# Kernel tuning notes

Measured on AMD Instinct MI355X. Metric: run time of the kernel, lower is better.

## Reference

```python
import jax, jax.numpy as jnp
import numpy as np

B, N, DIM, H = 16, 197, 768, 12
HD = DIM // H
SCALE = HD ** -0.5
T = 4 * B * N          # uncompressed new-token stream from the 4 frames
M = B * N + T          # cache tokens + new tokens (gather source length)
INNER = 64             # restoration MLP inner dim
FF = 4 * DIM

def _ln(x, g, b, eps=1e-5):
    m = jnp.mean(x, axis=-1, keepdims=True)
    v = jnp.var(x, axis=-1, keepdims=True)
    return (x - m) * jax.lax.rsqrt(v + eps) * g + b

def _quick_gelu(x):
    return x * jax.nn.sigmoid(1.702 * x)

def setup_inputs():
    key = jax.random.key(0)
    ks = jax.random.split(key, 16)
    s = 0.02
    return {
        'list_hidden_states': jax.random.normal(ks[0], (1, T, DIM), jnp.float32),
        'diff_pre_proj': jax.random.normal(ks[1], (4, B, N, DIM), jnp.float32),
        'hqkv_cache': jax.random.normal(ks[2], (4, B, N, DIM), jnp.float32),
        'ln1_g': jnp.ones((DIM,), jnp.float32), 'ln1_b': jnp.zeros((DIM,), jnp.float32),
        'wq': jax.random.normal(ks[3], (DIM, DIM), jnp.float32) * s, 'bq': jnp.zeros((DIM,), jnp.float32),
        'wk': jax.random.normal(ks[4], (DIM, DIM), jnp.float32) * s, 'bk': jnp.zeros((DIM,), jnp.float32),
        'wv': jax.random.normal(ks[5], (DIM, DIM), jnp.float32) * s, 'bv': jnp.zeros((DIM,), jnp.float32),
        'rest_w1': jax.random.normal(ks[6], (DIM, INNER), jnp.float32) * s,
        'rest_w2': jax.random.normal(ks[7], (INNER, 4 * DIM), jnp.float32) * s,
        'wo': jax.random.normal(ks[8], (DIM, DIM), jnp.float32) * s, 'bo': jnp.zeros((DIM,), jnp.float32),
        'ln2_g': jnp.ones((DIM,), jnp.float32), 'ln2_b': jnp.zeros((DIM,), jnp.float32),
        'fc1_w': jax.random.normal(ks[9], (DIM, FF), jnp.float32) * s, 'fc1_b': jnp.zeros((FF,), jnp.float32),
        'fc2_w': jax.random.normal(ks[10], (FF, DIM), jnp.float32) * s, 'fc2_b': jnp.zeros((DIM,), jnp.float32),
        'gather_idxs': jax.random.randint(ks[11], (4, B, N), 0, M),
        'reuse_map': jax.random.bernoulli(ks[12], 0.5, (4, B, N)),
    }

def _forward(list_hidden_states, diff_pre_proj, hqkv_cache,
             ln1_g, ln1_b, wq, bq, wk, bk, wv, bv,
             rest_w1, rest_w2, wo, bo, ln2_g, ln2_b,
             fc1_w, fc1_b, fc2_w, fc2_b, gather_idxs, reuse_map):
    h_cache, q_cache, k_cache, v_cache = hqkv_cache  # each [B,N,DIM]
    hs = list_hidden_states                          # [1,T,DIM]
    # layer_norm1 + QKV projection on the new tokens
    x = _ln(hs, ln1_g, ln1_b)
    q_new = x @ wq + bq
    k_new = x @ wk + bk
    v_new = x @ wv + bv
    # cache concat -> [M, DIM]
    h_p = jnp.concatenate([h_cache.reshape(-1, DIM), hs[0]], 0)
    q_p = jnp.concatenate([q_cache.reshape(-1, DIM), q_new[0]], 0)
    k_p = jnp.concatenate([k_cache.reshape(-1, DIM), k_new[0]], 0)
    v_p = jnp.concatenate([v_cache.reshape(-1, DIM), v_new[0]], 0)
    # index-based gather across the 4 frames -> [4,B,N,DIM]
    h_g = h_p[gather_idxs]
    q_g = q_p[gather_idxs]
    k_g = k_p[gather_idxs]
    v_g = v_p[gather_idxs]
    # restoration MLP on diffs, applied only at reused positions
    diff = jax.nn.gelu(diff_pre_proj @ rest_w1) @ rest_w2   # [4,B,N,4*DIM]
    hd, qd, kd, vd = jnp.split(diff, 4, axis=-1)
    m = reuse_map[..., None]
    h_g = h_g + jnp.where(m, hd, 0.0)
    q_g = q_g + jnp.where(m, qd, 0.0)
    k_g = k_g + jnp.where(m, kd, 0.0)
    v_g = v_g + jnp.where(m, vd, 0.0)
    # manual bmm-softmax-bmm attention over 4*B sequences
    FB = 4 * B
    q = q_g.reshape(FB, N, H, HD) * SCALE
    k = k_g.reshape(FB, N, H, HD)
    v = v_g.reshape(FB, N, H, HD)
    attn = jax.nn.softmax(jnp.einsum('bqhd,bkhd->bhqk', q, k), axis=-1)
    pre_proj = jnp.einsum('bhqk,bkhd->bqhd', attn, v).reshape(4, B, N, DIM)
    h_g = h_g.reshape(4, B, N, DIM)
    # last layer: keep only the CLS token
    h_cls = h_g[:, :, :1]
    pre_cls = pre_proj[:, :, :1]
    out = h_cls + (pre_cls @ wo + bo)
    resid = out
    out = _ln(out, ln2_g, ln2_b)
    out = _quick_gelu(out @ fc1_w + fc1_b) @ fc2_w + fc2_b  # CLIP MLP
    return resid + out   # [4,B,1,DIM]

def reference(list_hidden_states, diff_pre_proj, hqkv_cache,
              ln1_g, ln1_b, wq, bq, wk, bk, wv, bv,
              rest_w1, rest_w2, wo, bo, ln2_g, ln2_b,
              fc1_w, fc1_b, fc2_w, fc2_b, gather_idxs, reuse_map):
    return _forward(list_hidden_states, diff_pre_proj, hqkv_cache,
                    ln1_g, ln1_b, wq, bq, wk, bk, wv, bv,
                    rest_w1, rest_w2, wo, bo, ln2_g, ln2_b,
                    fc1_w, fc1_b, fc2_w, fc2_b, gather_idxs, reuse_map)
```

## Files before the change

kernel.cpp:

```cpp
#include <hip/hip_runtime.h>
#include <hip/hip_bf16.h>

#define TT 12608
#define NC 3152
#define DIM 768
#define NPOS 197
#define NH 12
#define HD 64
#define FB_N 64
#define FF 3072
#define INNER_D 64
#define NCOLS 1536

#define NB_TW  1728
#define NB_TW1 48
#define NB_S1  (NB_TW + NB_TW1 + TT)
#define NB_INN 99
#define NB_QF  6
#define NB_KV  1248
#define NB_S2  (NB_INN + NB_QF + NB_KV)

typedef __bf16 bf16x8 __attribute__((ext_vector_type(8)));
typedef float f32x4 __attribute__((ext_vector_type(4)));

__device__ inline float wred_sum(float v){
  #pragma unroll
  for (int o = 32; o > 0; o >>= 1) v += __shfl_down(v, o, 64);
  return v;
}
__device__ inline float wred_max(float v){
  #pragma unroll
  for (int o = 32; o > 0; o >>= 1) v = fmaxf(v, __shfl_down(v, o, 64));
  return v;
}

__device__ __forceinline__ void gl_lds16(const __bf16* g, __bf16* l) {
  __builtin_amdgcn_global_load_lds(
      (const __attribute__((address_space(1))) void*)g,
      (__attribute__((address_space(3))) void*)l, 16, 0, 0);
}

__global__ void detect_flag_kernel(const int* __restrict__ gidx, const unsigned char* __restrict__ rm,
                                   int* __restrict__ flag, int* __restrict__ det)
{
  int g = blockIdx.x * 256 + threadIdx.x;
  int la = 0, lb = 0;
  if (g < TT) {
    int idx = gidx[g];
    if (idx >= NC) flag[idx - NC] = 1;
    unsigned char v = rm[g];
    if (v) { if (g & 3) la = 1; else lb = 1; }
  }
  unsigned long long ba = __ballot(la != 0), bb = __ballot(lb != 0);
  if ((threadIdx.x & 63) == 0) {
    if (ba) atomicOr(&det[0], 1);
    if (bb) atomicOr(&det[1], 1);
  }
}

__launch_bounds__(1024)
__global__ void scan_kernel(const int* __restrict__ flag, const unsigned char* __restrict__ rm,
                            const int* __restrict__ det, unsigned char* __restrict__ mask,
                            int* __restrict__ rowlist, int* __restrict__ remap,
                            int* __restrict__ mrowlist, int* __restrict__ mremap,
                            int* __restrict__ mc)
{
  __shared__ int wsumA[16], wsumB[16];
  __shared__ int baseA, baseB;
  int t = threadIdx.x, lane = t & 63, wv = t >> 6;
  int mode = (!det[0]) ? 0 : (det[1] ? 1 : 2);
  if (t == 0) { baseA = 0; baseB = 0; }
  __syncthreads();
  for (int start = 0; start < TT; start += 1024) {
    int i = start + t;
    int fA = 0, fB = 0;
    if (i < TT) {
      fA = flag[i];
      unsigned char mb_;
      if (mode == 0)      mb_ = ((const int*)rm)[i] != 0;
      else if (mode == 1) mb_ = rm[i] != 0;
      else                mb_ = ((const float*)rm)[i] != 0.0f;
      mask[i] = mb_;
      fB = mb_;
    }
    unsigned long long mbA = __ballot(fA != 0);
    unsigned long long mbB = __ballot(fB != 0);
    int rankA = __popcll(mbA & ((1ULL << lane) - 1ULL));
    int rankB = __popcll(mbB & ((1ULL << lane) - 1ULL));
    if (lane == 0) { wsumA[wv] = __popcll(mbA); wsumB[wv] = __popcll(mbB); }
    __syncthreads();
    int woffA = 0, woffB = 0;
    for (int w2 = 0; w2 < wv; w2++) { woffA += wsumA[w2]; woffB += wsumB[w2]; }
    if (fA) { int pos = baseA + woffA + rankA; rowlist[pos] = i; remap[i] = pos; }
    if (fB) { int pos = baseB + woffB + rankB; mrowlist[pos] = i; mremap[i] = pos; }
    __syncthreads();
    if (t == 0) {
      int ta = 0, tb = 0;
      for (int w2 = 0; w2 < 16; w2++) { ta += wsumA[w2]; tb += wsumB[w2]; }
      baseA += ta; baseB += tb;
    }
    __syncthreads();
  }
  if (t == 0) { mc[0] = baseA; mc[1] = baseB; }
}

__launch_bounds__(256)
__global__ void stage1_kernel(const float* __restrict__ wk, const float* __restrict__ wvw,
                              const float* __restrict__ wq, const float* __restrict__ w1,
                              const float* __restrict__ hs,
                              const float* __restrict__ ln1g, const float* __restrict__ ln1b,
                              const int* __restrict__ rowlist, const int* __restrict__ mc,
                              __bf16* __restrict__ wcatT, __bf16* __restrict__ wqT,
                              __bf16* __restrict__ w1T, __bf16* __restrict__ xbf)
{
  __shared__ __align__(16) char pool[4352];
  int b = blockIdx.x, t = threadIdx.x;
  if (b < NB_TW) {
    float (*tile)[33] = (float(*)[33])pool;
    int bz = b / 576, rem = b % 576;
    int bx = rem % 24, by = rem / 24;
    int tx = t & 31, ty = t >> 5;
    const float* src = (bz == 0) ? wk : (bz == 1) ? wvw : wq;
    __bf16* dst = (bz == 0) ? wcatT : (bz == 1) ? (wcatT + (size_t)768 * DIM) : wqT;
    #pragma unroll
    for (int i = 0; i < 32; i += 8)
      tile[ty + i][tx] = src[(size_t)(by*32 + ty + i) * DIM + bx*32 + tx];
    __syncthreads();
    #pragma unroll
    for (int i = 0; i < 32; i += 8)
      dst[(size_t)(bx*32 + ty + i) * DIM + by*32 + tx] = (__bf16)tile[tx][ty + i];
    return;
  }
  if (b < NB_TW + NB_TW1) {
    float (*tile)[33] = (float(*)[33])pool;
    int rem = b - NB_TW;
    int bx = rem % 24, by = rem / 24;
    int tx = t & 31, ty = t >> 5;
    #pragma unroll
    for (int i = 0; i < 32; i += 8)
      tile[ty + i][tx] = w1[(size_t)(bx*32 + ty + i) * INNER_D + by*32 + tx];
    __syncthreads();
    #pragma unroll
    for (int i = 0; i < 32; i += 8)
      w1T[(size_t)(by*32 + ty + i) * DIM + bx*32 + tx] = (__bf16)tile[tx][ty + i];
    return;
  }
  int crow = b - NB_TW - NB_TW1;
  if (crow >= mc[0]) return;
  float* red = (float*)pool;
  int row = rowlist[crow];
  const float* x = hs + (size_t)row * DIM;
  float v0 = x[t], v1 = x[t + 256], v2 = x[t + 512];
  float s = wred_sum(v0 + v1 + v2);
  float q = wred_sum(v0*v0 + v1*v1 + v2*v2);
  int wv = t >> 6, ln = t & 63;
  if (ln == 0) { red[wv] = s; red[4 + wv] = q; }
  __syncthreads();
  float mean = (red[0]+red[1]+red[2]+red[3]) * (1.f/DIM);
  float var  = (red[4]+red[5]+red[6]+red[7]) * (1.f/DIM) - mean*mean;
  float rr = rsqrtf(var + 1e-5f);
  #pragma unroll
  for (int j = 0; j < 3; j++) {
    int c = t + j*256;
    float v = (j==0) ? v0 : (j==1) ? v1 : v2;
    xbf[(size_t)crow*DIM + c] = (__bf16)((v - mean) * rr * ln1g[c] + ln1b[c]);
  }
}

__launch_bounds__(512)
__global__ void stage2_kernel(const __bf16* __restrict__ xbf, const __bf16* __restrict__ wcatT,
                              const float* __restrict__ bk, const float* __restrict__ bv,
                              const float* __restrict__ dpp, const __bf16* __restrict__ w1T,
                              const __bf16* __restrict__ wqT,
                              const int* __restrict__ mrowlist, const int* __restrict__ mc,
                              const int* __restrict__ gidx, const int* __restrict__ remap,
                              __bf16* __restrict__ k_newc, __bf16* __restrict__ v_newc,
                              float* __restrict__ inner_c, float* __restrict__ qfresh)
{
  __shared__ __align__(16) char pool[65536];
  int b = blockIdx.x, t = threadIdx.x;
  int lane = t & 63, wid = t >> 6;
  int fr = lane & 15, fg = lane >> 4;

  if (b < NB_INN) {
    int mcnt = mc[1];
    int row0 = b * 128;
    if (row0 >= mcnt) return;
    typedef __bf16 (*tA_t)[40];
    tA_t As = (tA_t)pool;
    tA_t Bs = (tA_t)(pool + 10240);
    int* rlist = (int*)(pool + 15360);
    int wr = wid >> 1, wc = wid & 1;
    if (t < 128) rlist[t] = mrowlist[min(row0 + t, mcnt - 1)];
    __syncthreads();

    int lr = t >> 2, lc = (t & 3) << 3;
    const float* aG = dpp + (size_t)rlist[lr] * DIM + lc;
    int lrB = (t & 255) >> 2;
    const __bf16* bG = w1T + (size_t)lrB * DIM + lc;

    f32x4 acc[2][2];
    #pragma unroll
    for (int m = 0; m < 2; m++)
      #pragma unroll
      for (int n = 0; n < 2; n++) acc[m][n] = (f32x4){0.f, 0.f, 0.f, 0.f};

    for (int k0 = 0; k0 < DIM; k0 += 32) {
      float4 a0 = *(const float4*)(aG + k0);
      float4 a1 = *(const float4*)(aG + k0 + 4);
      bf16x8 av;
      av[0] = (__bf16)a0.x; av[1] = (__bf16)a0.y; av[2] = (__bf16)a0.z; av[3] = (__bf16)a0.w;
      av[4] = (__bf16)a1.x; av[5] = (__bf16)a1.y; av[6] = (__bf16)a1.z; av[7] = (__bf16)a1.w;
      *(bf16x8*)&As[lr][lc] = av;
      if (t < 256) *(bf16x8*)&Bs[lrB][lc] = *(const bf16x8*)(bG + k0);
      __syncthreads();
      bf16x8 af[2], bb[2];
      #pragma unroll
      for (int m = 0; m < 2; m++) af[m] = *(const bf16x8*)&As[wr*32 + m*16 + fr][fg << 3];
      #pragma unroll
      for (int n = 0; n < 2; n++) bb[n] = *(const bf16x8*)&Bs[wc*32 + n*16 + fr][fg << 3];
      #pragma unroll
      for (int m = 0; m < 2; m++)
        #pragma unroll
        for (int n = 0; n < 2; n++)
          acc[m][n] = __builtin_amdgcn_mfma_f32_16x16x32_bf16(af[m], bb[n], acc[m][n], 0, 0, 0);
      __syncthreads();
    }

    #pragma unroll
    for (int m = 0; m < 2; m++) {
      #pragma unroll
      for (int n = 0; n < 2; n++) {
        int col = wc*32 + n*16 + fr;
        int orow = row0 + wr*32 + m*16 + fg*4;
        #pragma unroll
        for (int r = 0; r < 4; r++) {
          int rr = orow + r;
          if (rr < mcnt) {
            float x = acc[m][n][r];
            float u = 0.7978845608028654f * (x + 0.044715f * x * x * x);
            inner_c[(size_t)rr*INNER_D + col] = 0.5f * x * (1.0f + tanhf(u));
          }
        }
      }
    }
    return;
  }

  if (b < NB_INN + NB_QF) {
    int col0 = (b - NB_INN) * 128;
    typedef __bf16 (*tA_t)[40];
    tA_t As = (tA_t)pool;
    tA_t Bs = (tA_t)(pool + 5632);
    int* rl = (int*)(pool + 16384);
    int wr = wid >> 2, wc = wid & 3;
    if (t < FB_N) {
      int idx = gidx[t * NPOS];
      rl[t] = (idx >= NC) ? remap[idx - NC] : -1;
    }
    __syncthreads();

    f32x4 acc[2][2];
    #pragma unroll
    for (int m = 0; m < 2; m++)
      #pragma unroll
      for (int n = 0; n < 2; n++) acc[m][n] = (f32x4){0.f, 0.f, 0.f, 0.f};

    int ar = (t & 255) >> 2, ac8 = (t & 3) << 3;
    int crow = (t < 256) ? rl[ar] : -1;
    int brw = t >> 2, bc8 = (t & 3) << 3;
    for (int k0 = 0; k0 < DIM; k0 += 32) {
      if (t < 256) {
        bf16x8 av = {};
        if (crow >= 0) av = *(const bf16x8*)(xbf + (size_t)crow*DIM + k0 + ac8);
        *(bf16x8*)&As[ar][ac8] = av;
      }
      *(bf16x8*)&Bs[brw][bc8] = *(const bf16x8*)(wqT + (size_t)(col0 + brw)*DIM + k0 + bc8);
      __syncthreads();
      bf16x8 af[2], bb[2];
      #pragma unroll
      for (int m = 0; m < 2; m++) af[m] = *(const bf16x8*)&As[wr*32 + m*16 + fr][fg << 3];
      #pragma unroll
      for (int n = 0; n < 2; n++) bb[n] = *(const bf16x8*)&Bs[wc*32 + n*16 + fr][fg << 3];
      #pragma unroll
      for (int m = 0; m < 2; m++)
        #pragma unroll
        for (int n = 0; n < 2; n++)
          acc[m][n] = __builtin_amdgcn_mfma_f32_16x16x32_bf16(af[m], bb[n], acc[m][n], 0, 0, 0);
      __syncthreads();
    }
    #pragma unroll
    for (int m = 0; m < 2; m++) {
      #pragma unroll
      for (int n = 0; n < 2; n++) {
        int col = col0 + wc*32 + n*16 + fr;
        int row = wr*32 + m*16 + fg*4;
        #pragma unroll
        for (int r = 0; r < 4; r++)
          qfresh[(size_t)(row + r)*DIM + col] = acc[m][n][r];
      }
    }
    return;
  }

  {
    int Mc = mc[0];
    int npanels = (Mc + 127) >> 7;
    int b2 = b - NB_INN - NB_QF;
    int xcd = b2 & 7, s2 = b2 >> 3;
    int panel = (s2 / 12) * 8 + xcd;
    if (panel >= npanels) return;
    int col0 = (s2 % 12) * 128;
    int row0 = panel * 128;
    char* poolA0 = pool;
    char* poolA1 = pool + 16384;
    char* poolB0 = pool + 32768;
    char* poolB1 = pool + 49152;
    int wr = wid >> 2, wc = wid & 3;

    int tr = t >> 3;
    int tc = (t & 7) << 4;
    int cbp = tc ^ ((tr & 7) << 4);
    const __bf16* aP[2];
    const __bf16* bP[2];
    #pragma unroll
    for (int c2 = 0; c2 < 2; c2++) {
      int r = c2*64 + tr;
      aP[c2] = xbf + (size_t)min(row0 + r, Mc - 1) * DIM + (cbp >> 1);
      bP[c2] = wcatT + (size_t)(col0 + r) * DIM + (cbp >> 1);
    }

    int rA[4], rB[2];
    #pragma unroll
    for (int m = 0; m < 4; m++) rA[m] = wr*64 + m*16 + fr;
    #pragma unroll
    for (int n = 0; n < 2; n++) rB[n] = wc*32 + n*16 + fr;
    int swzf = (fr & 7) << 4;

    f32x4 acc[4][2];
    #pragma unroll
    for (int m = 0; m < 4; m++)
      #pragma unroll
      for (int n = 0; n < 2; n++) acc[m][n] = (f32x4){0.f, 0.f, 0.f, 0.f};

    auto STAGE = [&](int s, char* dA, char* dB) {
      int k0 = s * 64;
      #pragma unroll
      for (int c2 = 0; c2 < 2; c2++) {
        gl_lds16(aP[c2] + k0, (__bf16*)(dA + c2*8192 + t*16));
        gl_lds16(bP[c2] + k0, (__bf16*)(dB + c2*8192 + t*16));
      }
    };

    STAGE(0, poolA0, poolB0);
    for (int s = 0; s < 12; s++) {
      char* curA = (s & 1) ? poolA1 : poolA0;
      char* curB = (s & 1) ? poolB1 : poolB0;
      if (s < 11) {
        STAGE(s + 1, (s & 1) ? poolA0 : poolA1, (s & 1) ? poolB0 : poolB1);
        asm volatile("s_waitcnt vmcnt(4)" ::: "memory");
      } else {
        asm volatile("s_waitcnt vmcnt(0)" ::: "memory");
      }
      __builtin_amdgcn_s_barrier();
      __builtin_amdgcn_sched_barrier(0);
      #pragma unroll
      for (int kk = 0; kk < 2; kk++) {
        int co = (kk*64 + (fg << 4)) ^ swzf;
        bf16x8 af[4], bb[2];
        #pragma unroll
        for (int m = 0; m < 4; m++) af[m] = *(const bf16x8*)(curA + rA[m]*128 + co);
        #pragma unroll
        for (int n = 0; n < 2; n++) bb[n] = *(const bf16x8*)(curB + rB[n]*128 + co);
        #pragma unroll
        for (int m = 0; m < 4; m++)
          #pragma unroll
          for (int n = 0; n < 2; n++)
            acc[m][n] = __builtin_amdgcn_mfma_f32_16x16x32_bf16(af[m], bb[n], acc[m][n], 0, 0, 0);
      }
      __builtin_amdgcn_sched_barrier(0);
      __builtin_amdgcn_s_barrier();
    }

    bool isK = (col0 < 768);
    const float* bias = isK ? bk : bv;
    __bf16* dst = isK ? k_newc : v_newc;
    int cbase = isK ? col0 : col0 - 768;
    __bf16* Ct = (__bf16*)pool;
    #pragma unroll
    for (int h = 0; h < 2; h++) {
      __syncthreads();
      if (wr == h) {
        #pragma unroll
        for (int n = 0; n < 2; n++) {
          int col = wc*32 + n*16 + fr;
          float bc = bias[cbase + col];
          #pragma unroll
          for (int m = 0; m < 4; m++) {
            int rl2 = m*16 + fg*4;
            #pragma unroll
            for (int r = 0; r < 4; r++)
              Ct[(rl2 + r)*128 + col] = (__bf16)(acc[m][n][r] + bc);
          }
        }
      }
      __syncthreads();
      #pragma unroll
      for (int c2 = 0; c2 < 2; c2++) {
        int o = c2*8192 + t*16;
        int rl2 = o >> 8;
        int cb = o & 255;
        int grow = row0 + h*64 + rl2;
        if (grow < Mc)
          *(uint4*)(dst + (size_t)grow*DIM + cbase + (cb >> 1)) = *(const uint4*)((char*)Ct + o);
      }
    }
  }
}

__launch_bounds__(256)
__global__ void cls_gather_kernel(const float* __restrict__ hs, const float* __restrict__ hqkv,
                                  const float* __restrict__ bq,
                                  const float* __restrict__ w2, const float* __restrict__ inner_c,
                                  const int* __restrict__ gidx, const unsigned char* __restrict__ mask,
                                  const int* __restrict__ mremap,
                                  float* __restrict__ h_cls, float* __restrict__ qbase)
{
  int fb = blockIdx.x, t = threadIdx.x;
  int g0 = fb * NPOS;
  int idx = gidx[g0];
  int m = mask[g0];
  const float* q_cache = hqkv + (size_t)NC * DIM;
  __shared__ float inn[INNER_D];
  if (t < INNER_D) inn[t] = m ? inner_c[(size_t)mremap[g0]*INNER_D + t] : 0.f;
  __syncthreads();
  bool fresh = idx >= NC;
  for (int c = t; c < DIM; c += 256) {
    float hv = fresh ? hs[(size_t)(idx - NC)*DIM + c] : hqkv[(size_t)idx*DIM + c];
    float qb = fresh ? bq[c] : q_cache[(size_t)idx*DIM + c];
    if (m) {
      float hd = 0.f, qd = 0.f;
      #pragma unroll 8
      for (int j = 0; j < INNER_D; j++) {
        float iv = inn[j];
        hd += iv * w2[(size_t)j*FF + c];
        qd += iv * w2[(size_t)j*FF + DIM + c];
      }
      hv += hd; qb += qd;
    }
    h_cls[(size_t)fb*DIM + c] = hv;
    qbase[(size_t)fb*DIM + c] = qb;
  }
}

__launch_bounds__(256)
__global__ void pgemm_kernel(const float* __restrict__ X, const float* __restrict__ W,
                             float* __restrict__ part, int N, int K, int kChunk)
{
  int t = threadIdx.x;
  int c = t & 63;
  int rq = t >> 6;
  int col0 = blockIdx.x * 64;
  int k0base = blockIdx.y * kChunk;
  __shared__ __align__(16) float Xs[64][68];
  float acc[16];
  #pragma unroll
  for (int i = 0; i < 16; i++) acc[i] = 0.f;
  for (int k0 = k0base; k0 < k0base + kChunk; k0 += 64) {
    #pragma unroll
    for (int j = 0; j < 4; j++) {
      int v = t + 256*j;
      int rr = v >> 4, cc = (v & 15) << 2;
      *(float4*)&Xs[rr][cc] = *(const float4*)&X[(size_t)rr*K + k0 + cc];
    }
    __syncthreads();
    const float* Wp = W + (size_t)k0*N + col0 + c;
    #pragma unroll 4
    for (int kk = 0; kk < 64; kk += 4) {
      float w0 = Wp[(size_t)(kk+0)*N];
      float w1 = Wp[(size_t)(kk+1)*N];
      float w2 = Wp[(size_t)(kk+2)*N];
      float w3 = Wp[(size_t)(kk+3)*N];
      #pragma unroll
      for (int r = 0; r < 16; r++) {
        float4 xv = *(const float4*)&Xs[rq*16 + r][kk];
        acc[r] += xv.x*w0 + xv.y*w1 + xv.z*w2 + xv.w*w3;
      }
    }
    __syncthreads();
  }
  #pragma unroll
  for (int r = 0; r < 16; r++)
    part[((size_t)blockIdx.y*64 + rq*16 + r)*N + col0 + c] = acc[r];
}

__launch_bounds__(512)
__global__ void attn_cls_kernel(const float* __restrict__ hqkv, const __bf16* __restrict__ k_newc,
                                const __bf16* __restrict__ v_newc, const float* __restrict__ w2,
                                const float* __restrict__ inner_c, const int* __restrict__ gidx,
                                const unsigned char* __restrict__ mask, const int* __restrict__ remap,
                                const int* __restrict__ mremap,
                                const float* __restrict__ qbase, const float* __restrict__ qfresh,
                                float* __restrict__ pre_cls)
{
  int bid = blockIdx.x;
  int fb = bid / NH, h = bid % NH;
  int t = threadIdx.x;
  int lane = t & 63, wv = t >> 6;
  const float* k_cache = hqkv + (size_t)2 * NC * DIM;
  const float* v_cache = hqkv + (size_t)3 * NC * DIM;
  __shared__ float q0[HD], w2q[INNER_D], tj[INNER_D];
  __shared__ float p[200];
  __shared__ int sidx[200];
  __shared__ int smg[200];
  __shared__ float red[16];
  __shared__ float pacc[8][64];
  if (t < HD) {
    size_t qoff = (size_t)fb*DIM + h*HD + t;
    q0[t] = (qbase[qoff] + qfresh[qoff]) * 0.125f;
  }
  int tt = t - 64;
  if (tt >= 0 && tt < NPOS) {
    int g = fb * NPOS + tt;
    int idx = gidx[g];
    if (idx >= NC) idx = NC + remap[idx - NC];
    sidx[tt] = idx;
    smg[tt] = mask[g] ? mremap[g] : -1;
  }
  __syncthreads();
  {
    int j = t >> 3, dg = t & 7;
    const float* wr = w2 + (size_t)j*FF + 2*DIM + h*HD + dg*8;
    float4 a = *(const float4*)wr, b = *(const float4*)(wr + 4);
    const float* q = &q0[dg*8];
    float s = a.x*q[0] + a.y*q[1] + a.z*q[2] + a.w*q[3]
            + b.x*q[4] + b.y*q[5] + b.z*q[6] + b.w*q[7];
    s += __shfl_xor(s, 1); s += __shfl_xor(s, 2); s += __shfl_xor(s, 4);
    if (dg == 0) w2q[j] = s;
  }
  __syncthreads();
  #pragma unroll
  for (int it = 0; it < 4; it++) {
    int n = it*64 + wv*8 + (lane >> 3);
    int dg = lane & 7;
    if (n < NPOS) {
      int idx = sidx[n], mg = smg[n];
      const float* q = &q0[dg*8];
      float s = 0.f;
      if (idx >= NC) {
        bf16x8 kv = *(const bf16x8*)(k_newc + (size_t)(idx - NC)*DIM + h*HD + dg*8);
        #pragma unroll
        for (int j = 0; j < 8; j++) s += q[j] * (float)kv[j];
      } else {
        const float* kr = k_cache + (size_t)idx*DIM + h*HD + dg*8;
        float4 a = *(const float4*)kr, b = *(const float4*)(kr + 4);
        s = a.x*q[0] + a.y*q[1] + a.z*q[2] + a.w*q[3]
          + b.x*q[4] + b.y*q[5] + b.z*q[6] + b.w*q[7];
      }
      if (mg >= 0) {
        const float* ir = inner_c + (size_t)mg*INNER_D + dg*8;
        float4 a = *(const float4*)ir, b = *(const float4*)(ir + 4);
        const float* wq8 = &w2q[dg*8];
        s += a.x*wq8[0] + a.y*wq8[1] + a.z*wq8[2] + a.w*wq8[3]
           + b.x*wq8[4] + b.y*wq8[5] + b.z*wq8[6] + b.w*wq8[7];
      }
      s += __shfl_xor(s, 1); s += __shfl_xor(s, 2); s += __shfl_xor(s, 4);
      if (dg == 0) p[n] = s;
    }
  }
  __syncthreads();
  float lm = (t < NPOS) ? p[t] : -1e30f;
  lm = wred_max(lm);
  if (lane == 0) red[wv] = lm;
  __syncthreads();
  float mx = red[0];
  #pragma unroll
  for (int w = 1; w < 8; w++) mx = fmaxf(mx, red[w]);
  float lp = 0.f;
  if (t < NPOS) { lp = __expf(p[t] - mx); p[t] = lp; }
  float ls = wred_sum(lp);
  if (lane == 0) red[8 + wv] = ls;
  __syncthreads();
  float inv = red[8];
  #pragma unroll
  for (int w = 1; w < 8; w++) inv += red[8 + w];
  inv = 1.0f / inv;
  float tp = 0.f;
  for (int n = wv; n < NPOS; n += 8) {
    int mg = smg[n];
    if (mg >= 0) tp += p[n] * inner_c[(size_t)mg*INNER_D + lane];
  }
  pacc[wv][lane] = tp;
  __syncthreads();
  if (t < INNER_D) tj[t] = pacc[0][t] + pacc[1][t] + pacc[2][t] + pacc[3][t]
                         + pacc[4][t] + pacc[5][t] + pacc[6][t] + pacc[7][t];
  __syncthreads();
  float va = 0.f;
  for (int n = wv; n < NPOS; n += 8) {
    float pn = p[n];
    int idx = sidx[n];
    float vvv;
    if (idx >= NC) vvv = (float)v_newc[(size_t)(idx - NC)*DIM + h*HD + lane];
    else           vvv = v_cache[(size_t)idx*DIM + h*HD + lane];
    va += pn * vvv;
  }
  __syncthreads();
  pacc[wv][lane] = va;
  __syncthreads();
  if (t < HD) {
    float o = pacc[0][t] + pacc[1][t] + pacc[2][t] + pacc[3][t]
            + pacc[4][t] + pacc[5][t] + pacc[6][t] + pacc[7][t];
    const float* wv2 = w2 + 3*DIM + h*HD + t;
    float dd = 0.f;
    for (int j = 0; j < INNER_D; j++) dd += tj[j] * wv2[(size_t)j*FF];
    pre_cls[(size_t)fb*DIM + h*HD + t] = (o + dd) * inv;
  }
}

__launch_bounds__(256)
__global__ void reduce_wo_ln_kernel(const float* __restrict__ partW, const float* __restrict__ bo,
                                    const float* __restrict__ h_cls, const float* __restrict__ g,
                                    const float* __restrict__ b, float* __restrict__ out0,
                                    float* __restrict__ yln)
{
  int row = blockIdx.x, t = threadIdx.x;
  float v[3];
  #pragma unroll
  for (int j = 0; j < 3; j++) {
    int c = t + j*256;
    float s = h_cls[(size_t)row*DIM + c] + bo[c];
    #pragma unroll
    for (int ks = 0; ks < 12; ks++) s += partW[((size_t)ks*FB_N + row)*DIM + c];
    v[j] = s;
    out0[(size_t)row*DIM + c] = s;
  }
  float sm = wred_sum(v[0] + v[1] + v[2]);
  float sq = wred_sum(v[0]*v[0] + v[1]*v[1] + v[2]*v[2]);
  __shared__ float red[8];
  int wv = t >> 6, ln = t & 63;
  if (ln == 0) { red[wv] = sm; red[4 + wv] = sq; }
  __syncthreads();
  float mean = (red[0]+red[1]+red[2]+red[3]) * (1.f/DIM);
  float var  = (red[4]+red[5]+red[6]+red[7]) * (1.f/DIM) - mean*mean;
  float rr = rsqrtf(var + 1e-5f);
  #pragma unroll
  for (int j = 0; j < 3; j++) {
    int c = t + j*256;
    yln[(size_t)row*DIM + c] = (v[j] - mean) * rr * g[c] + b[c];
  }
}

__global__ void reduce_gelu_kernel(const float* __restrict__ partF1, const float* __restrict__ b1,
                                   float* __restrict__ t1)
{
  int i = blockIdx.x * 256 + threadIdx.x;
  int c = i % FF;
  float v = b1[c];
  #pragma unroll
  for (int s = 0; s < 6; s++) v += partF1[(size_t)s*FB_N*FF + i];
  t1[i] = v / (1.0f + __expf(-1.702f * v));
}

__global__ void final_reduce_kernel(const float* __restrict__ out0, const float* __restrict__ b2,
                                    const float* __restrict__ partF2, float* __restrict__ dout)
{
  int i = blockIdx.x * 256 + threadIdx.x;
  int c = i % DIM;
  float v = out0[i] + b2[c];
  #pragma unroll
  for (int s = 0; s < 24; s++) v += partF2[(size_t)s*FB_N*DIM + i];
  dout[i] = v;
}

extern "C" void kernel_launch(void* const* d_in, const int* in_sizes, int n_in,
                              void* d_out, int out_size, void* d_ws, size_t ws_size,
                              hipStream_t stream)
{
  const float* hs   = (const float*)d_in[0];
  const float* dpp  = (const float*)d_in[1];
  const float* hqkv = (const float*)d_in[2];
  const float* ln1g = (const float*)d_in[3];
  const float* ln1b = (const float*)d_in[4];
  const float* wq   = (const float*)d_in[5];
  const float* bq   = (const float*)d_in[6];
  const float* wk   = (const float*)d_in[7];
  const float* bk   = (const float*)d_in[8];
  const float* wvw  = (const float*)d_in[9];
  const float* bv   = (const float*)d_in[10];
  const float* w1   = (const float*)d_in[11];
  const float* w2   = (const float*)d_in[12];
  const float* wo   = (const float*)d_in[13];
  const float* bo   = (const float*)d_in[14];
  const float* ln2g = (const float*)d_in[15];
  const float* ln2b = (const float*)d_in[16];
  const float* fc1w = (const float*)d_in[17];
  const float* fc1b = (const float*)d_in[18];
  const float* fc2w = (const float*)d_in[19];
  const float* fc2b = (const float*)d_in[20];
  const int*   gidx = (const int*)d_in[21];
  const unsigned char* rmap = (const unsigned char*)d_in[22];
  float* outp = (float*)d_out;

  char* ws = (char*)d_ws;
  size_t off = 0;
  auto alloc = [&](size_t bytes) { void* p = ws + off; off += (bytes + 255) & ~(size_t)255; return p; };
  unsigned char* mask = (unsigned char*)alloc(TT);
  int* flag     = (int*)alloc((size_t)TT * 4);
  int* mc       = (int*)alloc(256);
  int* rowlist  = (int*)alloc((size_t)TT * 4);
  int* remap    = (int*)alloc((size_t)TT * 4);
  int* mrowlist = (int*)alloc((size_t)TT * 4);
  int* mremap   = (int*)alloc((size_t)TT * 4);
  __bf16* xbf    = (__bf16*)alloc((size_t)TT * DIM * 2);
  __bf16* wcatT  = (__bf16*)alloc((size_t)NCOLS * DIM * 2);
  __bf16* wqT    = (__bf16*)alloc((size_t)DIM * DIM * 2);
  __bf16* w1T    = (__bf16*)alloc((size_t)INNER_D * DIM * 2);
  __bf16* k_newc = (__bf16*)alloc((size_t)TT * DIM * 2);
  __bf16* v_newc = (__bf16*)alloc((size_t)TT * DIM * 2);
  float* inner_c = (float*)alloc((size_t)TT * INNER_D * 4);
  float* qfresh  = (float*)alloc((size_t)FB_N * DIM * 4);
  float* h_cls  = (float*)alloc((size_t)FB_N * DIM * 4);
  float* qbase  = (float*)alloc((size_t)FB_N * DIM * 4);
  float* precls = (float*)alloc((size_t)FB_N * DIM * 4);
  float* out0   = (float*)alloc((size_t)FB_N * DIM * 4);
  float* yln    = (float*)alloc((size_t)FB_N * DIM * 4);
  float* t1     = (float*)alloc((size_t)FB_N * FF * 4);
  float* partW  = (float*)alloc((size_t)12 * FB_N * DIM * 4);
  float* partF1 = (float*)alloc((size_t)6  * FB_N * FF  * 4);
  float* partF2 = (float*)alloc((size_t)24 * FB_N * DIM * 4);
  (void)ws_size; (void)in_sizes; (void)n_in; (void)out_size;

  hipMemsetAsync(flag, 0, (size_t)TT * 4 + 256, stream);
  detect_flag_kernel<<<(TT + 255) / 256, 256, 0, stream>>>(gidx, rmap, flag, mc + 2);
  scan_kernel<<<1, 1024, 0, stream>>>(flag, rmap, mc + 2, mask, rowlist, remap,
                                      mrowlist, mremap, mc);
  stage1_kernel<<<NB_S1, 256, 0, stream>>>(wk, wvw, wq, w1, hs, ln1g, ln1b, rowlist, mc,
                                           wcatT, wqT, w1T, xbf);
  stage2_kernel<<<NB_S2, 512, 0, stream>>>(xbf, wcatT, bk, bv, dpp, w1T, wqT, mrowlist, mc,
                                           gidx, remap, k_newc, v_newc, inner_c, qfresh);
  cls_gather_kernel<<<FB_N, 256, 0, stream>>>(hs, hqkv, bq, w2, inner_c, gidx, mask,
                                              mremap, h_cls, qbase);
  attn_cls_kernel<<<FB_N * NH, 512, 0, stream>>>(hqkv, k_newc, v_newc, w2, inner_c, gidx, mask,
                                                 remap, mremap, qbase, qfresh, precls);
  pgemm_kernel<<<dim3(12, 12), 256, 0, stream>>>(precls, wo, partW, DIM, DIM, 64);
  reduce_wo_ln_kernel<<<FB_N, 256, 0, stream>>>(partW, bo, h_cls, ln2g, ln2b, out0, yln);
  pgemm_kernel<<<dim3(48, 6), 256, 0, stream>>>(yln, fc1w, partF1, FF, DIM, 128);
  reduce_gelu_kernel<<<768, 256, 0, stream>>>(partF1, fc1b, t1);
  pgemm_kernel<<<dim3(12, 24), 256, 0, stream>>>(t1, fc2w, partF2, DIM, FF, 128);
  final_reduce_kernel<<<192, 256, 0, stream>>>(out0, fc2b, partF2, outp);
}
```

Before: 176.7 us.

## Replace single-block scan with multi-block atomic compaction and batch pgemm weight loads

The one-block, 1024-thread serial scan over all tokens is replaced by a grid of 256-thread blocks. Each block ballots its flags locally and reserves its output range with an atomicAdd on the global counters. This removes a long serialized kernel from the critical path. The compacted row lists are no longer in index order, though remap stays consistent with them. Separately, the partial GEMM inner loop now loads 16 weight values ahead before the FMA loop, so more global loads are in flight per thread.

```diff
diff --git a/kernel.cpp b/kernel.cpp
--- a/kernel.cpp
+++ b/kernel.cpp
@@ -58,50 +58,45 @@
   }
 }
 
-__launch_bounds__(1024)
-__global__ void scan_kernel(const int* __restrict__ flag, const unsigned char* __restrict__ rm,
-                            const int* __restrict__ det, unsigned char* __restrict__ mask,
-                            int* __restrict__ rowlist, int* __restrict__ remap,
-                            int* __restrict__ mrowlist, int* __restrict__ mremap,
-                            int* __restrict__ mc)
-{
-  __shared__ int wsumA[16], wsumB[16];
-  __shared__ int baseA, baseB;
+__launch_bounds__(256)
+__global__ void compact_kernel(const int* __restrict__ flag, const unsigned char* __restrict__ rm,
+                               const int* __restrict__ det, unsigned char* __restrict__ mask,
+                               int* __restrict__ rowlist, int* __restrict__ remap,
+                               int* __restrict__ mrowlist, int* __restrict__ mremap,
+                               int* __restrict__ mc)
+{
+  __shared__ int wsumA[4], wsumB[4];
+  __shared__ int baseA_s, baseB_s;
   int t = threadIdx.x, lane = t & 63, wv = t >> 6;
+  int i = blockIdx.x * 256 + t;
   int mode = (!det[0]) ? 0 : (det[1] ? 1 : 2);
-  if (t == 0) { baseA = 0; baseB = 0; }
-  __syncthreads();
-  for (int start = 0; start < TT; start += 1024) {
-    int i = start + t;
-    int fA = 0, fB = 0;
-    if (i < TT) {
-      fA = flag[i];
-      unsigned char mb_;
-      if (mode == 0)      mb_ = ((const int*)rm)[i] != 0;
-      else if (mode == 1) mb_ = rm[i] != 0;
-      else                mb_ = ((const float*)rm)[i] != 0.0f;
-      mask[i] = mb_;
-      fB = mb_;
-    }
-    unsigned long long mbA = __ballot(fA != 0);
-    unsigned long long mbB = __ballot(fB != 0);
-    int rankA = __popcll(mbA & ((1ULL << lane) - 1ULL));
-    int rankB = __popcll(mbB & ((1ULL << lane) - 1ULL));
-    if (lane == 0) { wsumA[wv] = __popcll(mbA); wsumB[wv] = __popcll(mbB); }
-    __syncthreads();
-    int woffA = 0, woffB = 0;
-    for (int w2 = 0; w2 < wv; w2++) { woffA += wsumA[w2]; woffB += wsumB[w2]; }
-    if (fA) { int pos = baseA + woffA + rankA; rowlist[pos] = i; remap[i] = pos; }
-    if (fB) { int pos = baseB + woffB + rankB; mrowlist[pos] = i; mremap[i] = pos; }
-    __syncthreads();
-    if (t == 0) {
-      int ta = 0, tb = 0;
-      for (int w2 = 0; w2 < 16; w2++) { ta += wsumA[w2]; tb += wsumB[w2]; }
-      baseA += ta; baseB += tb;
-    }
-    __syncthreads();
-  }
-  if (t == 0) { mc[0] = baseA; mc[1] = baseB; }
+  int fA = 0, fB = 0;
+  if (i < TT) {
+    fA = flag[i];
+    unsigned char mb_;
+    if (mode == 0)      mb_ = ((const int*)rm)[i] != 0;
+    else if (mode == 1) mb_ = rm[i] != 0;
+    else                mb_ = ((const float*)rm)[i] != 0.0f;
+    mask[i] = mb_;
+    fB = mb_;
+  }
+  unsigned long long mbA = __ballot(fA != 0);
+  unsigned long long mbB = __ballot(fB != 0);
+  int rankA = __popcll(mbA & ((1ULL << lane) - 1ULL));
+  int rankB = __popcll(mbB & ((1ULL << lane) - 1ULL));
+  if (lane == 0) { wsumA[wv] = __popcll(mbA); wsumB[wv] = __popcll(mbB); }
+  __syncthreads();
+  if (t == 0) {
+    int ta = wsumA[0] + wsumA[1] + wsumA[2] + wsumA[3];
+    int tb = wsumB[0] + wsumB[1] + wsumB[2] + wsumB[3];
+    baseA_s = ta ? atomicAdd(&mc[0], ta) : 0;
+    baseB_s = tb ? atomicAdd(&mc[1], tb) : 0;
+  }
+  __syncthreads();
+  int woffA = 0, woffB = 0;
+  for (int w = 0; w < wv; w++) { woffA += wsumA[w]; woffB += wsumB[w]; }
+  if (fA) { int pos = baseA_s + woffA + rankA; rowlist[pos] = i; remap[i] = pos; }
+  if (fB) { int pos = baseB_s + woffB + rankB; mrowlist[pos] = i; mremap[i] = pos; }
 }
 
 __launch_bounds__(256)
@@ -475,16 +470,18 @@
     }
     __syncthreads();
     const float* Wp = W + (size_t)k0*N + col0 + c;
-    #pragma unroll 4
-    for (int kk = 0; kk < 64; kk += 4) {
-      float w0 = Wp[(size_t)(kk+0)*N];
-      float w1 = Wp[(size_t)(kk+1)*N];
-      float w2 = Wp[(size_t)(kk+2)*N];
-      float w3 = Wp[(size_t)(kk+3)*N];
-      #pragma unroll
-      for (int r = 0; r < 16; r++) {
-        float4 xv = *(const float4*)&Xs[rq*16 + r][kk];
-        acc[r] += xv.x*w0 + xv.y*w1 + xv.z*w2 + xv.w*w3;
+    #pragma unroll
+    for (int kk0 = 0; kk0 < 64; kk0 += 16) {
+      float w[16];
+      #pragma unroll
+      for (int u = 0; u < 16; u++) w[u] = Wp[(size_t)(kk0 + u)*N];
+      #pragma unroll
+      for (int u = 0; u < 16; u += 4) {
+        #pragma unroll
+        for (int r = 0; r < 16; r++) {
+          float4 xv = *(const float4*)&Xs[rq*16 + r][kk0 + u];
+          acc[r] += xv.x*w[u] + xv.y*w[u+1] + xv.z*w[u+2] + xv.w*w[u+3];
+        }
       }
     }
     __syncthreads();
@@ -732,8 +729,8 @@
 
   hipMemsetAsync(flag, 0, (size_t)TT * 4 + 256, stream);
   detect_flag_kernel<<<(TT + 255) / 256, 256, 0, stream>>>(gidx, rmap, flag, mc + 2);
-  scan_kernel<<<1, 1024, 0, stream>>>(flag, rmap, mc + 2, mask, rowlist, remap,
-                                      mrowlist, mremap, mc);
+  compact_kernel<<<(TT + 255) / 256, 256, 0, stream>>>(flag, rmap, mc + 2, mask,
+                                                       rowlist, remap, mrowlist, mremap, mc);
   stage1_kernel<<<NB_S1, 256, 0, stream>>>(wk, wvw, wq, w1, hs, ln1g, ln1b, rowlist, mc,
                                            wcatT, wqT, w1T, xbf);
   stage2_kernel<<<NB_S2, 512, 0, stream>>>(xbf, wcatT, bk, bv, dpp, w1T, wqT, mrowlist, mc,
```

After: 152.7 us (median of 3 runs). 13.6% less time.
